# Kernel tuning notes

Hardware: AMD Instinct MI355X
Metric: run time of the kernel (lower is better)

Reference implementation:

```python
import jax, jax.numpy as jnp
import numpy as np


def setup_inputs() -> dict:
    key = jax.random.key(0)
    ks = jax.random.split(key, 5)
    B, T, I, H = 32, 512, 1024, 1024
    s = 1.0 / np.sqrt(I + H)  # fan-in scaling similar to nn.Linear init
    return {
        "x": jax.random.normal(ks[0], (B, T, I), dtype=jnp.float32),
        "Wf": jax.random.normal(ks[1], (I + H, H), dtype=jnp.float32) * s,
        "bf": jnp.zeros((H,), dtype=jnp.float32),
        "Wi": jax.random.normal(ks[2], (I + H, H), dtype=jnp.float32) * s,
        "bi": jnp.zeros((H,), dtype=jnp.float32),
        "Wo": jax.random.normal(ks[3], (I + H, H), dtype=jnp.float32) * s,
        "bo": jnp.zeros((H,), dtype=jnp.float32),
        "Wc": jax.random.normal(ks[4], (I + H, H), dtype=jnp.float32) * s,
        "bc": jnp.zeros((H,), dtype=jnp.float32),
    }


def reference(x, Wf, bf, Wi, bi, Wo, bo, Wc, bc):
    B, T, I = x.shape
    H = Wf.shape[1]
    # Fuse the four gate projections into one GEMM per step: [I+H, 4H]
    W = jnp.concatenate([Wf, Wi, Wo, Wc], axis=1)
    b = jnp.concatenate([bf, bi, bo, bc], axis=0)
    xt = jnp.transpose(x, (1, 0, 2))  # [T, B, I]

    def step(carry, x_i):
        h, c = carry
        inp = jnp.concatenate([x_i, h], axis=1)          # [B, I+H]
        gates = inp @ W + b                               # [B, 4H]
        f, i, o, g = jnp.split(gates, 4, axis=1)
        f = jax.nn.sigmoid(f)
        i = jax.nn.sigmoid(i)
        o = jax.nn.sigmoid(o)
        g = jnp.tanh(g)
        c = f * c + i * g
        h = o * jnp.tanh(c)
        return (h, c), (h, c)

    h0 = jnp.zeros((B, H), dtype=x.dtype)
    c0 = jnp.zeros((B, H), dtype=x.dtype)
    (h_last, _), (h_states, c_states) = jax.lax.scan(step, (h0, c0), xt)
    # h_states, c_states: [T, B, H] (stacked equivalents of the python lists)
    return h_last, h_states, c_states
```

## Files before the change

### kernel.cpp

```cpp
#include <hip/hip_runtime.h>
#include <hip/hip_bf16.h>

typedef __attribute__((ext_vector_type(8))) short short8b;
typedef __attribute__((ext_vector_type(4))) float f32x4;

#define B_   32
#define T_   512
#define I_   1024
#define H_   1024
#define K_   2048
#define NB   256
#define NTHR 128
#define BH   (B_ * H_)
#define HLAST (B_ * H_)
#define TBH ((long)T_ * B_ * H_)
#define SC_SYS __HIP_MEMORY_SCOPE_SYSTEM
#define MAGIC 0x5AB00000u

__device__ __forceinline__ unsigned short f2bf(float f) {
  union { float f; unsigned u; } c; c.f = f;
  unsigned r = (c.u + 0x7FFFu + ((c.u >> 16) & 1u)) >> 16;
  return (unsigned short)r;
}

__device__ __forceinline__ float sig_(float x)  { return 1.0f / (1.0f + __expf(-x)); }
__device__ __forceinline__ float tanh_(float x) { return 1.0f - 2.0f / (__expf(2.0f * x) + 1.0f); }

__device__ __forceinline__ unsigned long long ld64sys(const void* p) {
  return __hip_atomic_load((const unsigned long long*)p, __ATOMIC_RELAXED, SC_SYS);
}

__global__ void convert_x_kernel(const float* __restrict__ x, unsigned short* __restrict__ xb) {
  long vid = (long)blockIdx.x * blockDim.x + threadIdx.x;
  long o = vid * 4;
  if (o >= (long)T_ * B_ * I_) return;
  int i  = (int)(o & (I_ - 1));
  long bt = o >> 10;
  int b  = (int)(bt & (B_ - 1));
  int t  = (int)(bt >> 5);
  float4 v = *reinterpret_cast<const float4*>(x + (((long)b * T_ + t) << 10) + i);
  ushort4 pk;
  pk.x = f2bf(v.x); pk.y = f2bf(v.y); pk.z = f2bf(v.z); pk.w = f2bf(v.w);
  *reinterpret_cast<ushort4*>(xb + o) = pk;
}

template <bool XBF16>
__global__ __launch_bounds__(NTHR, 1)
void lstm_kernel(const unsigned short* __restrict__ xb, const float* __restrict__ xf,
                 const float* __restrict__ Wf, const float* __restrict__ Wi,
                 const float* __restrict__ Wo, const float* __restrict__ Wc,
                 const float* __restrict__ bfp, const float* __restrict__ bip,
                 const float* __restrict__ bop, const float* __restrict__ bcp,
                 float* __restrict__ out, char* __restrict__ hseqp,
                 unsigned* __restrict__ flags)
{
  __shared__ unsigned short Wl[16 * 2048];
  const int tid = threadIdx.x;
  const int bid = blockIdx.x;
  const int j0  = bid * 4;

  {
    const float* Wg[4] = {Wf, Wi, Wo, Wc};
    for (int g = 0; g < 4; ++g) {
      const float* Wp = Wg[g] + j0;
      for (int k = tid; k < K_; k += NTHR) {
        float4 w = *reinterpret_cast<const float4*>(Wp + (long)k * H_);
        float wv[4] = {w.x, w.y, w.z, w.w};
        #pragma unroll
        for (int cj = 0; cj < 4; ++cj) {
          int n = g * 4 + cj;
          int byteoff = n * 4096 + ((2 * k) ^ ((n & 7) << 4));
          *reinterpret_cast<unsigned short*>(reinterpret_cast<char*>(Wl) + byteoff) = f2bf(wv[cj]);
        }
      }
    }
  }
  __syncthreads();

  __builtin_amdgcn_fence(__ATOMIC_ACQUIRE, "agent");

  const int lane = tid & 63;
  const int m    = tid >> 6;
  const int lr   = lane & 15;
  const int lg   = lane >> 4;
  const int b    = m * 16 + lr;
  const int cj   = lane & 3;
  const int gb0  = m * 16 + lg * 4;

  const float bias_f = bfp[j0 + cj];
  const float bias_i = bip[j0 + cj];
  const float bias_o = bop[j0 + cj];
  const float bias_g = bcp[j0 + cj];

  float creg[4] = {0.f, 0.f, 0.f, 0.f};

  const char* WlB   = reinterpret_cast<const char*>(Wl);
  const int colbase = lr * 4096;
  const int swz     = (lr & 7) << 4;

  auto xpart = [&](int t, f32x4& a0, f32x4& a1) {
    a0 = f32x4{0.f, 0.f, 0.f, 0.f};
    a1 = f32x4{0.f, 0.f, 0.f, 0.f};
    if (XBF16) {
      const unsigned short* aptr = xb + (((long)(t * B_ + b)) << 10) + lg * 8;
      #pragma unroll
      for (int it = 0; it < 32; ++it) {
        short8b a  = *reinterpret_cast<const short8b*>(aptr + it * 32);
        short8b bb = *reinterpret_cast<const short8b*>(WlB + colbase + ((it * 64 + lg * 16) ^ swz));
        if (it & 1) a1 = __builtin_amdgcn_mfma_f32_16x16x32_bf16(a, bb, a1, 0, 0, 0);
        else        a0 = __builtin_amdgcn_mfma_f32_16x16x32_bf16(a, bb, a0, 0, 0, 0);
      }
    } else {
      const float* aptr = xf + ((long)b * T_ + t) * I_ + lg * 8;
      #pragma unroll
      for (int it = 0; it < 32; ++it) {
        float4 v0 = *reinterpret_cast<const float4*>(aptr + it * 32);
        float4 v1 = *reinterpret_cast<const float4*>(aptr + it * 32 + 4);
        union { __hip_bfloat162 h2[4]; short8b v; } cv;
        cv.h2[0] = __float22bfloat162_rn(float2{v0.x, v0.y});
        cv.h2[1] = __float22bfloat162_rn(float2{v0.z, v0.w});
        cv.h2[2] = __float22bfloat162_rn(float2{v1.x, v1.y});
        cv.h2[3] = __float22bfloat162_rn(float2{v1.z, v1.w});
        short8b bb = *reinterpret_cast<const short8b*>(WlB + colbase + ((it * 64 + lg * 16) ^ swz));
        if (it & 1) a1 = __builtin_amdgcn_mfma_f32_16x16x32_bf16(cv.v, bb, a1, 0, 0, 0);
        else        a0 = __builtin_amdgcn_mfma_f32_16x16x32_bf16(cv.v, bb, a0, 0, 0, 0);
      }
    }
  };

  f32x4 xa0, xa1;
  xpart(0, xa0, xa1);

  for (int t = 0; t < T_; ++t) {
    f32x4 a0 = xa0, a1 = xa1;

    if (t > 0) {
      {
        const unsigned exp32 = MAGIC | (unsigned)(t - 1);
        const unsigned long long pat =
            ((unsigned long long)exp32 << 32) | (unsigned long long)exp32;
        const unsigned long long* fb =
            reinterpret_cast<const unsigned long long*>(flags + (long)(t - 1) * 512) + lane * 4;
        while (true) {
          unsigned long long f0 = ld64sys(fb);
          unsigned long long f1 = ld64sys(fb + 1);
          unsigned long long f2 = ld64sys(fb + 2);
          unsigned long long f3 = ld64sys(fb + 3);
          if (__all((f0 == pat) & (f1 == pat) & (f2 == pat) & (f3 == pat))) break;
        }
      }
      asm volatile("" ::: "memory");

      const char* hb = hseqp + ((long)(t - 1) << 16) + m * 128 + lr * 8 + lg * 512;
      unsigned long long u0[8][2], u1[8][2];
      auto issue = [&](int g, unsigned long long (&u)[8][2]) {
        #pragma unroll
        for (int f = 0; f < 8; ++f) {
          const char* p = hb + ((g * 8 + f) * 8) * 256;
          u[f][0] = *reinterpret_cast<const unsigned long long*>(p);
          u[f][1] = *reinterpret_cast<const unsigned long long*>(p + 256);
        }
      };
      auto domfma = [&](int g, unsigned long long (&u)[8][2]) {
        #pragma unroll
        for (int f = 0; f < 8; ++f) {
          const int it = g * 8 + f;
          union { unsigned long long q[2]; short8b v; } cv;
          cv.q[0] = u[f][0]; cv.q[1] = u[f][1];
          short8b bb = *reinterpret_cast<const short8b*>(
              WlB + colbase + ((2048 + it * 64 + lg * 16) ^ swz));
          if (it & 1) a1 = __builtin_amdgcn_mfma_f32_16x16x32_bf16(cv.v, bb, a1, 0, 0, 0);
          else        a0 = __builtin_amdgcn_mfma_f32_16x16x32_bf16(cv.v, bb, a0, 0, 0, 0);
        }
      };
      issue(0, u0);
      issue(1, u1);
      domfma(0, u0); issue(2, u0);
      domfma(1, u1); issue(3, u1);
      domfma(2, u0);
      domfma(3, u1);
    }

    f32x4 acc = a0 + a1;

    float gate[4][4];
    #pragma unroll
    for (int g = 0; g < 4; ++g) {
      const int src = lg * 16 + g * 4 + cj;
      #pragma unroll
      for (int r = 0; r < 4; ++r) gate[g][r] = __shfl(acc[r], src, 64);
    }

    float hv[4];
    #pragma unroll
    for (int r = 0; r < 4; ++r) {
      float fg = sig_(gate[0][r] + bias_f);
      float ig = sig_(gate[1][r] + bias_i);
      float og = sig_(gate[2][r] + bias_o);
      float gg = tanh_(gate[3][r] + bias_g);
      float c  = fg * creg[r] + ig * gg;
      creg[r]  = c;
      hv[r]    = og * tanh_(c);
    }

    if (t < T_ - 1) {
      const int src = ((lane >> 4) << 4) | (lane & 3);
      float hr0 = __shfl(hv[0], src, 64);
      float hr1 = __shfl(hv[1], src, 64);
      float hr2 = __shfl(hv[2], src, 64);
      float hr3 = __shfl(hv[3], src, 64);
      const int rsel = (lane >> 2) & 3;
      float v = (rsel == 0) ? hr0 : (rsel == 1) ? hr1 : (rsel == 2) ? hr2 : hr3;
      unsigned short hs = f2bf(v);
      __hip_atomic_store(
          reinterpret_cast<unsigned short*>(hseqp + ((long)t << 16) + bid * 256 + m * 128 + lane * 2),
          hs, __ATOMIC_RELAXED, SC_SYS);
      asm volatile("s_waitcnt vmcnt(0)" ::: "memory");
      if (lane == 0)
        __hip_atomic_store(&flags[(long)t * 512 + bid * 2 + m], MAGIC | (unsigned)t,
                           __ATOMIC_RELAXED, SC_SYS);
    }

    if ((lane & 12) == 0) {
      #pragma unroll
      for (int r = 0; r < 4; ++r) {
        const int row  = gb0 + r;
        const int colj = j0 + cj;
        const long oh  = (long)(t * B_ + row) * H_ + colj;
        out[HLAST + oh]       = hv[r];
        out[HLAST + TBH + oh] = creg[r];
        if (t == T_ - 1) out[(long)row * H_ + colj] = hv[r];
      }
    }

    if (t + 1 < T_) xpart(t + 1, xa0, xa1);
  }
}

__global__ void lstm_step_fallback_kernel(int t,
    const float* __restrict__ xf,
    const float* __restrict__ Wf, const float* __restrict__ Wi,
    const float* __restrict__ Wo, const float* __restrict__ Wc,
    const float* __restrict__ bfp, const float* __restrict__ bip,
    const float* __restrict__ bop, const float* __restrict__ bcp,
    float* __restrict__ out, unsigned short* __restrict__ hbuf)
{
  const int tid  = threadIdx.x;
  const int bid  = blockIdx.x;
  const int lane = tid & 63;
  const int m    = tid >> 6;
  const int lr   = lane & 15;
  const int lg   = lane >> 4;
  const int b    = m * 16 + lr;
  const int cj   = lane & 3;
  const int j0   = bid * 4;
  const int gb0  = m * 16 + lg * 4;

  const unsigned short* hcur = hbuf + (t & 1) * BH;
  f32x4 a0 = {0.f, 0.f, 0.f, 0.f};
  f32x4 a1 = {0.f, 0.f, 0.f, 0.f};

  const int g    = lr >> 2;
  const int colg = j0 + (lr & 3);
  const float* Wg = (g == 0) ? Wf : (g == 1) ? Wi : (g == 2) ? Wo : Wc;
  const float* axf = xf + ((long)b * T_ + t) * I_ + lg * 8;
  const unsigned short* ah = hcur + (b << 10) + lg * 8;
  #pragma unroll 4
  for (int it = 0; it < 32; ++it) {
    const int k0 = it * 32 + lg * 8;
    short8b a, bb;
    #pragma unroll
    for (int e = 0; e < 8; ++e) {
      a[e]  = (short)f2bf(axf[it * 32 + e]);
      bb[e] = (short)f2bf(Wg[(size_t)(k0 + e) * H_ + colg]);
    }
    if (it & 1) a1 = __builtin_amdgcn_mfma_f32_16x16x32_bf16(a, bb, a1, 0, 0, 0);
    else        a0 = __builtin_amdgcn_mfma_f32_16x16x32_bf16(a, bb, a0, 0, 0, 0);
  }
  #pragma unroll 4
  for (int it = 0; it < 32; ++it) {
    const int k0 = 1024 + it * 32 + lg * 8;
    short8b a = *reinterpret_cast<const short8b*>(ah + it * 32);
    short8b bb;
    #pragma unroll
    for (int e = 0; e < 8; ++e)
      bb[e] = (short)f2bf(Wg[(size_t)(k0 + e) * H_ + colg]);
    if (it & 1) a1 = __builtin_amdgcn_mfma_f32_16x16x32_bf16(a, bb, a1, 0, 0, 0);
    else        a0 = __builtin_amdgcn_mfma_f32_16x16x32_bf16(a, bb, a0, 0, 0, 0);
  }
  f32x4 acc = a0 + a1;

  float gate[4][4];
  #pragma unroll
  for (int gg = 0; gg < 4; ++gg) {
    const int src = lg * 16 + gg * 4 + cj;
    #pragma unroll
    for (int r = 0; r < 4; ++r) gate[gg][r] = __shfl(acc[r], src, 64);
  }

  if ((lane & 12) == 0) {
    const int col = j0 + cj;
    const float bias_f = bfp[col];
    const float bias_i = bip[col];
    const float bias_o = bop[col];
    const float bias_g = bcp[col];
    #pragma unroll
    for (int r = 0; r < 4; ++r) {
      const int row = gb0 + r;
      float cp = (t == 0) ? 0.f
               : out[HLAST + TBH + (long)((t - 1) * B_ + row) * H_ + col];
      float fg = sig_(gate[0][r] + bias_f);
      float ig = sig_(gate[1][r] + bias_i);
      float og = sig_(gate[2][r] + bias_o);
      float gv = tanh_(gate[3][r] + bias_g);
      float c  = fg * cp + ig * gv;
      float hv = og * tanh_(c);
      const long oh = (long)(t * B_ + row) * H_ + col;
      out[HLAST + oh]       = hv;
      out[HLAST + TBH + oh] = c;
      hbuf[((t + 1) & 1) * BH + row * H_ + col] = f2bf(hv);
      if (t == T_ - 1) out[(long)row * H_ + col] = hv;
    }
  }
}

extern "C" void kernel_launch(void* const* d_in, const int* in_sizes, int n_in,
                              void* d_out, int out_size, void* d_ws, size_t ws_size,
                              hipStream_t stream) {
  const float* x   = (const float*)d_in[0];
  const float* Wf  = (const float*)d_in[1];
  const float* bf_ = (const float*)d_in[2];
  const float* Wi  = (const float*)d_in[3];
  const float* bi_ = (const float*)d_in[4];
  const float* Wo  = (const float*)d_in[5];
  const float* bo_ = (const float*)d_in[6];
  const float* Wc  = (const float*)d_in[7];
  const float* bc_ = (const float*)d_in[8];
  float* out = (float*)d_out;

  const size_t hseq_bytes  = (size_t)T_ * 65536;
  const size_t flags_bytes = (size_t)T_ * 512 * 4;
  const size_t xb_bytes    = (size_t)T_ * B_ * I_ * 2;
  const bool has_hseq = ws_size >= hseq_bytes + flags_bytes;
  const bool has_xb   = ws_size >= hseq_bytes + flags_bytes + xb_bytes;

  if (has_hseq) {
    char* hseqp        = (char*)d_ws;
    unsigned* flags    = (unsigned*)((char*)d_ws + hseq_bytes);
    unsigned short* xb = (unsigned short*)((char*)d_ws + hseq_bytes + flags_bytes);

    (void)hipMemsetAsync(flags, 0, flags_bytes, stream);

    if (has_xb) {
      const int total_vec = T_ * B_ * I_ / 4;
      convert_x_kernel<<<dim3(total_vec / 256), dim3(256), 0, stream>>>(x, xb);
      lstm_kernel<true><<<dim3(NB), dim3(NTHR), 0, stream>>>(
          xb, x, Wf, Wi, Wo, Wc, bf_, bi_, bo_, bc_, out, hseqp, flags);
    } else {
      lstm_kernel<false><<<dim3(NB), dim3(NTHR), 0, stream>>>(
          xb, x, Wf, Wi, Wo, Wc, bf_, bi_, bo_, bc_, out, hseqp, flags);
    }
  } else {
    unsigned short* hbuf = (unsigned short*)d_ws;
    (void)hipMemsetAsync(hbuf, 0, (size_t)2 * BH * 2, stream);
    for (int t = 0; t < T_; ++t)
      lstm_step_fallback_kernel<<<dim3(NB), dim3(NTHR), 0, stream>>>(
          t, x, Wf, Wi, Wo, Wc, bf_, bi_, bo_, bc_, out, hbuf);
  }
}
```

Before: 3.004 ms.

## Use one wave per block with two batch chunks and double-buffered h slab

Each block now runs a single 64-thread wavefront that handles both 16-row batch chunks in sequence, with separate flags per chunk. The h exchange moves from a per-timestep buffer to a small double-buffered slab that stays cache-resident, and the input projection for the next step runs between the h store and the flag release. This lets the second chunk's recurrent work overlap the first chunk's flag propagation and cuts the workspace footprint. In exchange each block has half the threads, so the MFMA work per wave doubles and the serial critical path per step may get longer. The two-slot reuse is only safe if no block can get two steps ahead of the others.

```diff
diff --git a/kernel.cpp b/kernel.cpp
--- a/kernel.cpp
+++ b/kernel.cpp
@@ -10,12 +10,13 @@
 #define H_   1024
 #define K_   2048
 #define NB   256
-#define NTHR 128
+#define NTHR 64
 #define BH   (B_ * H_)
 #define HLAST (B_ * H_)
 #define TBH ((long)T_ * B_ * H_)
 #define SC_SYS __HIP_MEMORY_SCOPE_SYSTEM
 #define MAGIC 0x5AB00000u
+#define SLABSUB 32768
 
 __device__ __forceinline__ unsigned short f2bf(float f) {
   union { float f; unsigned u; } c; c.f = f;
@@ -51,7 +52,7 @@
                  const float* __restrict__ Wo, const float* __restrict__ Wc,
                  const float* __restrict__ bfp, const float* __restrict__ bip,
                  const float* __restrict__ bop, const float* __restrict__ bcp,
-                 float* __restrict__ out, char* __restrict__ hseqp,
+                 float* __restrict__ out, char* __restrict__ slab,
                  unsigned* __restrict__ flags)
 {
   __shared__ unsigned short Wl[16 * 2048];
@@ -76,33 +77,30 @@
     }
   }
   __syncthreads();
-
   __builtin_amdgcn_fence(__ATOMIC_ACQUIRE, "agent");
 
   const int lane = tid & 63;
-  const int m    = tid >> 6;
   const int lr   = lane & 15;
   const int lg   = lane >> 4;
-  const int b    = m * 16 + lr;
   const int cj   = lane & 3;
-  const int gb0  = m * 16 + lg * 4;
 
   const float bias_f = bfp[j0 + cj];
   const float bias_i = bip[j0 + cj];
   const float bias_o = bop[j0 + cj];
   const float bias_g = bcp[j0 + cj];
 
-  float creg[4] = {0.f, 0.f, 0.f, 0.f};
+  float creg[2][4] = {{0.f,0.f,0.f,0.f},{0.f,0.f,0.f,0.f}};
 
   const char* WlB   = reinterpret_cast<const char*>(Wl);
   const int colbase = lr * 4096;
   const int swz     = (lr & 7) << 4;
 
-  auto xpart = [&](int t, f32x4& a0, f32x4& a1) {
+  auto xpart = [&](int t, int ch, f32x4& a0, f32x4& a1) {
     a0 = f32x4{0.f, 0.f, 0.f, 0.f};
     a1 = f32x4{0.f, 0.f, 0.f, 0.f};
+    const int row = ch * 16 + lr;
     if (XBF16) {
-      const unsigned short* aptr = xb + (((long)(t * B_ + b)) << 10) + lg * 8;
+      const unsigned short* aptr = xb + (((long)(t * B_ + row)) << 10) + lg * 8;
       #pragma unroll
       for (int it = 0; it < 32; ++it) {
         short8b a  = *reinterpret_cast<const short8b*>(aptr + it * 32);
@@ -111,7 +109,7 @@
         else        a0 = __builtin_amdgcn_mfma_f32_16x16x32_bf16(a, bb, a0, 0, 0, 0);
       }
     } else {
-      const float* aptr = xf + ((long)b * T_ + t) * I_ + lg * 8;
+      const float* aptr = xf + ((long)row * T_ + t) * I_ + lg * 8;
       #pragma unroll
       for (int it = 0; it < 32; ++it) {
         float4 v0 = *reinterpret_cast<const float4*>(aptr + it * 32);
@@ -128,112 +126,116 @@
     }
   };
 
-  f32x4 xa0, xa1;
-  xpart(0, xa0, xa1);
+  f32x4 xa[2][2];
+  xpart(0, 0, xa[0][0], xa[0][1]);
+  xpart(0, 1, xa[1][0], xa[1][1]);
+
+  float hv[2][4];
 
   for (int t = 0; t < T_; ++t) {
-    f32x4 a0 = xa0, a1 = xa1;
-
-    if (t > 0) {
-      {
+    #pragma unroll
+    for (int ch = 0; ch < 2; ++ch) {
+      f32x4 a0 = xa[ch][0], a1 = xa[ch][1];
+
+      if (t > 0) {
         const unsigned exp32 = MAGIC | (unsigned)(t - 1);
         const unsigned long long pat =
             ((unsigned long long)exp32 << 32) | (unsigned long long)exp32;
-        const unsigned long long* fb =
-            reinterpret_cast<const unsigned long long*>(flags + (long)(t - 1) * 512) + lane * 4;
+        const unsigned long long* fb = reinterpret_cast<const unsigned long long*>(
+            flags + (((t - 1) & 1) * 2 + ch) * 256) + lane * 2;
         while (true) {
           unsigned long long f0 = ld64sys(fb);
           unsigned long long f1 = ld64sys(fb + 1);
-          unsigned long long f2 = ld64sys(fb + 2);
-          unsigned long long f3 = ld64sys(fb + 3);
-          if (__all((f0 == pat) & (f1 == pat) & (f2 == pat) & (f3 == pat))) break;
+          if (__all((f0 == pat) & (f1 == pat))) break;
         }
-      }
-      asm volatile("" ::: "memory");
-
-      const char* hb = hseqp + ((long)(t - 1) << 16) + m * 128 + lr * 8 + lg * 512;
-      unsigned long long u0[8][2], u1[8][2];
-      auto issue = [&](int g, unsigned long long (&u)[8][2]) {
+        asm volatile("" ::: "memory");
+
+        const char* hb = slab + (((t - 1) & 1) * 2 + ch) * SLABSUB + lr * 8 + lg * 256;
+        unsigned long long u0[8][2], u1[8][2];
+        auto issue = [&](int g, unsigned long long (&u)[8][2]) {
+          #pragma unroll
+          for (int f = 0; f < 8; ++f) {
+            const char* p = hb + ((g * 8 + f) * 8) * 128;
+            u[f][0] = ld64sys(p);
+            u[f][1] = ld64sys(p + 128);
+          }
+        };
+        auto domfma = [&](int g, unsigned long long (&u)[8][2]) {
+          #pragma unroll
+          for (int f = 0; f < 8; ++f) {
+            const int it = g * 8 + f;
+            union { unsigned long long q[2]; short8b v; } cv;
+            cv.q[0] = u[f][0]; cv.q[1] = u[f][1];
+            short8b bb = *reinterpret_cast<const short8b*>(
+                WlB + colbase + ((2048 + it * 64 + lg * 16) ^ swz));
+            if (it & 1) a1 = __builtin_amdgcn_mfma_f32_16x16x32_bf16(cv.v, bb, a1, 0, 0, 0);
+            else        a0 = __builtin_amdgcn_mfma_f32_16x16x32_bf16(cv.v, bb, a0, 0, 0, 0);
+          }
+        };
+        issue(0, u0);
+        issue(1, u1);
+        domfma(0, u0); issue(2, u0);
+        domfma(1, u1); issue(3, u1);
+        domfma(2, u0);
+        domfma(3, u1);
+      }
+
+      f32x4 acc = a0 + a1;
+
+      float gate[4][4];
+      #pragma unroll
+      for (int g = 0; g < 4; ++g) {
+        const int src = lg * 16 + g * 4 + cj;
         #pragma unroll
-        for (int f = 0; f < 8; ++f) {
-          const char* p = hb + ((g * 8 + f) * 8) * 256;
-          u[f][0] = *reinterpret_cast<const unsigned long long*>(p);
-          u[f][1] = *reinterpret_cast<const unsigned long long*>(p + 256);
+        for (int r = 0; r < 4; ++r) gate[g][r] = __shfl(acc[r], src, 64);
+      }
+      #pragma unroll
+      for (int r = 0; r < 4; ++r) {
+        float fg = sig_(gate[0][r] + bias_f);
+        float ig = sig_(gate[1][r] + bias_i);
+        float og = sig_(gate[2][r] + bias_o);
+        float gg = tanh_(gate[3][r] + bias_g);
+        float c  = fg * creg[ch][r] + ig * gg;
+        creg[ch][r] = c;
+        hv[ch][r]   = og * tanh_(c);
+      }
+
+      if (t < T_ - 1) {
+        const int src = ((lane >> 4) << 4) | (lane & 3);
+        float hr0 = __shfl(hv[ch][0], src, 64);
+        float hr1 = __shfl(hv[ch][1], src, 64);
+        float hr2 = __shfl(hv[ch][2], src, 64);
+        float hr3 = __shfl(hv[ch][3], src, 64);
+        const int rsel = (lane >> 2) & 3;
+        float v = (rsel == 0) ? hr0 : (rsel == 1) ? hr1 : (rsel == 2) ? hr2 : hr3;
+        __hip_atomic_store(
+            reinterpret_cast<unsigned short*>(
+                slab + ((t & 1) * 2 + ch) * SLABSUB + bid * 128 + lane * 2),
+            f2bf(v), __ATOMIC_RELAXED, SC_SYS);
+
+        xpart(t + 1, ch, xa[ch][0], xa[ch][1]);
+
+        asm volatile("s_waitcnt vmcnt(0)" ::: "memory");
+        if (lane == 0)
+          __hip_atomic_store(&flags[((t & 1) * 2 + ch) * 256 + bid],
+                             MAGIC | (unsigned)t, __ATOMIC_RELAXED, SC_SYS);
+      }
+    }
+
+    if ((lane & 12) == 0) {
+      #pragma unroll
+      for (int ch = 0; ch < 2; ++ch) {
+        #pragma unroll
+        for (int r = 0; r < 4; ++r) {
+          const int row  = ch * 16 + lg * 4 + r;
+          const int colj = j0 + cj;
+          const long oh  = (long)(t * B_ + row) * H_ + colj;
+          out[HLAST + oh]       = hv[ch][r];
+          out[HLAST + TBH + oh] = creg[ch][r];
+          if (t == T_ - 1) out[(long)row * H_ + colj] = hv[ch][r];
         }
-      };
-      auto domfma = [&](int g, unsigned long long (&u)[8][2]) {
-        #pragma unroll
-        for (int f = 0; f < 8; ++f) {
-          const int it = g * 8 + f;
-          union { unsigned long long q[2]; short8b v; } cv;
-          cv.q[0] = u[f][0]; cv.q[1] = u[f][1];
-          short8b bb = *reinterpret_cast<const short8b*>(
-              WlB + colbase + ((2048 + it * 64 + lg * 16) ^ swz));
-          if (it & 1) a1 = __builtin_amdgcn_mfma_f32_16x16x32_bf16(cv.v, bb, a1, 0, 0, 0);
-          else        a0 = __builtin_amdgcn_mfma_f32_16x16x32_bf16(cv.v, bb, a0, 0, 0, 0);
-        }
-      };
-      issue(0, u0);
-      issue(1, u1);
-      domfma(0, u0); issue(2, u0);
-      domfma(1, u1); issue(3, u1);
-      domfma(2, u0);
-      domfma(3, u1);
-    }
-
-    f32x4 acc = a0 + a1;
-
-    float gate[4][4];
-    #pragma unroll
-    for (int g = 0; g < 4; ++g) {
-      const int src = lg * 16 + g * 4 + cj;
-      #pragma unroll
-      for (int r = 0; r < 4; ++r) gate[g][r] = __shfl(acc[r], src, 64);
-    }
-
-    float hv[4];
-    #pragma unroll
-    for (int r = 0; r < 4; ++r) {
-      float fg = sig_(gate[0][r] + bias_f);
-      float ig = sig_(gate[1][r] + bias_i);
-      float og = sig_(gate[2][r] + bias_o);
-      float gg = tanh_(gate[3][r] + bias_g);
-      float c  = fg * creg[r] + ig * gg;
-      creg[r]  = c;
-      hv[r]    = og * tanh_(c);
-    }
-
-    if (t < T_ - 1) {
-      const int src = ((lane >> 4) << 4) | (lane & 3);
-      float hr0 = __shfl(hv[0], src, 64);
-      float hr1 = __shfl(hv[1], src, 64);
-      float hr2 = __shfl(hv[2], src, 64);
-      float hr3 = __shfl(hv[3], src, 64);
-      const int rsel = (lane >> 2) & 3;
-      float v = (rsel == 0) ? hr0 : (rsel == 1) ? hr1 : (rsel == 2) ? hr2 : hr3;
-      unsigned short hs = f2bf(v);
-      __hip_atomic_store(
-          reinterpret_cast<unsigned short*>(hseqp + ((long)t << 16) + bid * 256 + m * 128 + lane * 2),
-          hs, __ATOMIC_RELAXED, SC_SYS);
-      asm volatile("s_waitcnt vmcnt(0)" ::: "memory");
-      if (lane == 0)
-        __hip_atomic_store(&flags[(long)t * 512 + bid * 2 + m], MAGIC | (unsigned)t,
-                           __ATOMIC_RELAXED, SC_SYS);
-    }
-
-    if ((lane & 12) == 0) {
-      #pragma unroll
-      for (int r = 0; r < 4; ++r) {
-        const int row  = gb0 + r;
-        const int colj = j0 + cj;
-        const long oh  = (long)(t * B_ + row) * H_ + colj;
-        out[HLAST + oh]       = hv[r];
-        out[HLAST + TBH + oh] = creg[r];
-        if (t == T_ - 1) out[(long)row * H_ + colj] = hv[r];
-      }
-    }
-
-    if (t + 1 < T_) xpart(t + 1, xa0, xa1);
+      }
+    }
   }
 }
 
@@ -338,16 +340,16 @@
   const float* bc_ = (const float*)d_in[8];
   float* out = (float*)d_out;
 
-  const size_t hseq_bytes  = (size_t)T_ * 65536;
-  const size_t flags_bytes = (size_t)T_ * 512 * 4;
+  const size_t slab_bytes  = (size_t)4 * SLABSUB;
+  const size_t flags_bytes = (size_t)4 * 256 * 4;
   const size_t xb_bytes    = (size_t)T_ * B_ * I_ * 2;
-  const bool has_hseq = ws_size >= hseq_bytes + flags_bytes;
-  const bool has_xb   = ws_size >= hseq_bytes + flags_bytes + xb_bytes;
-
-  if (has_hseq) {
-    char* hseqp        = (char*)d_ws;
-    unsigned* flags    = (unsigned*)((char*)d_ws + hseq_bytes);
-    unsigned short* xb = (unsigned short*)((char*)d_ws + hseq_bytes + flags_bytes);
+  const bool has_slab = ws_size >= slab_bytes + flags_bytes;
+  const bool has_xb   = ws_size >= slab_bytes + flags_bytes + xb_bytes;
+
+  if (has_slab) {
+    char* slab         = (char*)d_ws;
+    unsigned* flags    = (unsigned*)((char*)d_ws + slab_bytes);
+    unsigned short* xb = (unsigned short*)((char*)d_ws + slab_bytes + flags_bytes);
 
     (void)hipMemsetAsync(flags, 0, flags_bytes, stream);
 
@@ -355,16 +357,16 @@
       const int total_vec = T_ * B_ * I_ / 4;
       convert_x_kernel<<<dim3(total_vec / 256), dim3(256), 0, stream>>>(x, xb);
       lstm_kernel<true><<<dim3(NB), dim3(NTHR), 0, stream>>>(
-          xb, x, Wf, Wi, Wo, Wc, bf_, bi_, bo_, bc_, out, hseqp, flags);
+          xb, x, Wf, Wi, Wo, Wc, bf_, bi_, bo_, bc_, out, slab, flags);
     } else {
       lstm_kernel<false><<<dim3(NB), dim3(NTHR), 0, stream>>>(
-          xb, x, Wf, Wi, Wo, Wc, bf_, bi_, bo_, bc_, out, hseqp, flags);
+          xb, x, Wf, Wi, Wo, Wc, bf_, bi_, bo_, bc_, out, slab, flags);
     }
   } else {
     unsigned short* hbuf = (unsigned short*)d_ws;
     (void)hipMemsetAsync(hbuf, 0, (size_t)2 * BH * 2, stream);
     for (int t = 0; t < T_; ++t)
-      lstm_step_fallback_kernel<<<dim3(NB), dim3(NTHR), 0, stream>>>(
+      lstm_step_fallback_kernel<<<dim3(NB), dim3(128), 0, stream>>>(
           t, x, Wf, Wi, Wo, Wc, bf_, bi_, bo_, bc_, out, hbuf);
   }
 }
```

Result: slower. 6.301 ms (+109.7%).
